# Performance work log

Hardware: AMD Instinct MI355X
Metric: run time of the kernel (lower is better)

Reference implementation:

```python
import jax, jax.numpy as jnp
import numpy as np

N_NODES = 50000
N_EDGES = 600000
BAG = 16
VOCAB = 10000
EMB = 128
HID = 128
N_CLASSES = 10
N_GRAPHS = 512
PAD_IDX = 1


def setup_inputs() -> dict:
    key = jax.random.key(0)
    ks = jax.random.split(key, 12)
    x_tokens = jax.random.randint(ks[0], (N_NODES, BAG), 0, VOCAB)
    src = jax.random.randint(ks[1], (N_EDGES,), 0, N_NODES)
    dst = jax.random.randint(ks[2], (N_EDGES,), 0, N_NODES)
    edge_index = jnp.stack([src, dst])
    batch = jnp.sort(jax.random.randint(ks[3], (N_NODES,), 0, N_GRAPHS))
    # rows 0,1 are zero in the original (weights[2:] filled from pretrained vectors)
    emb_table = (jax.random.normal(ks[4], (VOCAB, EMB)) * 0.02).at[:2].set(0.0)
    s = 1.0 / np.sqrt(EMB)
    w1_l = jax.random.normal(ks[5], (HID, EMB)) * s
    b1 = jnp.zeros((HID,), jnp.float32)
    w1_r = jax.random.normal(ks[6], (HID, EMB)) * s
    w2_l = jax.random.normal(ks[7], (HID, HID)) * s
    b2 = jnp.zeros((HID,), jnp.float32)
    w2_r = jax.random.normal(ks[8], (HID, HID)) * s
    w_out = jax.random.normal(ks[9], (N_CLASSES, HID)) * s
    b_out = jnp.zeros((N_CLASSES,), jnp.float32)
    return {"x_tokens": x_tokens, "edge_index": edge_index, "batch": batch,
            "emb_table": emb_table, "w1_l": w1_l, "b1": b1, "w1_r": w1_r,
            "w2_l": w2_l, "b2": b2, "w2_r": w2_r, "w_out": w_out, "b_out": b_out}


def _embedding_bag_mean(tokens, table):
    # nn.EmbeddingBag mode='mean' with padding_idx: padding tokens excluded from mean
    emb = table[tokens]                                  # [N, BAG, D]
    mask = (tokens != PAD_IDX)[..., None].astype(table.dtype)
    total = jnp.sum(emb * mask, axis=1)                  # [N, D]
    cnt = jnp.clip(jnp.sum(mask, axis=1), 1.0)           # [N, 1]
    return total / cnt


def _sage_conv(x, src, dst, w_l, b_l, w_r):
    # PyG SAGEConv: lin_l(mean_{j in N(i)} x_j) + lin_r(x_i); lin_r has no bias
    n = x.shape[0]
    msg_sum = jax.ops.segment_sum(x[src], dst, num_segments=n)           # [N, D]
    deg = jax.ops.segment_sum(jnp.ones((src.shape[0], 1), x.dtype), dst,
                              num_segments=n)                             # [N, 1]
    aggr = msg_sum / jnp.clip(deg, 1.0)
    return aggr @ w_l.T + b_l + x @ w_r.T


def reference(x_tokens, edge_index, batch, emb_table, w1_l, b1, w1_r,
              w2_l, b2, w2_r, w_out, b_out):
    src, dst = edge_index[0], edge_index[1]
    x = _embedding_bag_mean(x_tokens, emb_table)                 # [N, EMB]
    x = jax.nn.relu(_sage_conv(x, src, dst, w1_l, b1, w1_r))     # [N, HID]
    x = jax.nn.relu(_sage_conv(x, src, dst, w2_l, b2, w2_r))     # [N, HID]
    # global_mean_pool over graph ids
    g_sum = jax.ops.segment_sum(x, batch, num_segments=N_GRAPHS)
    g_cnt = jax.ops.segment_sum(jnp.ones((x.shape[0], 1), x.dtype), batch,
                                num_segments=N_GRAPHS)
    g = g_sum / jnp.clip(g_cnt, 1.0)                             # [G, HID]
    return g @ w_out.T + b_out                                   # [G, C]
```

## Files before the change

kernel.cpp:

```cpp
#include <hip/hip_runtime.h>
#include <hip/hip_bf16.h>

#define NN 50000
#define NE 600000
#define BAG 16
#define EMB 128
#define HID 128
#define NC 10
#define NG 512
#define PAD_IDX 1
#define VOCAB 10000
#define SLOTS 64
#define TPAIRS (VOCAB * EMB / 2)
#define WPAIRS (4 * HID * EMB / 2)
#define EMVB (NN / 16)
#define NCH1 293
#define RANGES 125
#define RNODES 400
#define QCAP 6400
#define NTILES ((NN + 127) / 128)

typedef __attribute__((ext_vector_type(8))) short v8s;
typedef __attribute__((ext_vector_type(4))) float v4f;

__device__ __forceinline__ float bflo(unsigned u) { return __uint_as_float(u << 16); }
__device__ __forceinline__ float bfhi(unsigned u) { return __uint_as_float(u & 0xffff0000u); }
__device__ __forceinline__ unsigned short f2bf(float f) {
    unsigned u = __float_as_uint(f);
    return (unsigned short)((u + 0x7fffu + ((u >> 16) & 1u)) >> 16);
}
__device__ __forceinline__ void acc8(float* a, v8s v) {
    unsigned* u = (unsigned*)&v;
#pragma unroll
    for (int j = 0; j < 4; j++) {
        a[2 * j] += bflo(u[j]);
        a[2 * j + 1] += bfhi(u[j]);
    }
}

__global__ void k_conv(const float* __restrict__ t, unsigned short* __restrict__ tb,
                       const float* __restrict__ w1l, const float* __restrict__ w1r,
                       const float* __restrict__ w2l, const float* __restrict__ w2r,
                       unsigned short* __restrict__ wbf, int* __restrict__ qtail,
                       float* __restrict__ gsum, float* __restrict__ gcnt) {
    int i = blockIdx.x * blockDim.x + threadIdx.x;
    if (i < RANGES) qtail[i] = 0;
    if (i < NG * HID) gsum[i] = 0.f;
    if (i < NG) gcnt[i] = 0.f;
    if (i < TPAIRS) {
        float2 v = *(const float2*)(t + (size_t)i * 2);
        unsigned lo = f2bf(v.x), hi = f2bf(v.y);
        *(unsigned*)(tb + (size_t)i * 2) = lo | (hi << 16);
    } else if (i < TPAIRS + WPAIRS) {
        int j = i - TPAIRS;
        int k = j * 2;
        int arr = k >> 14;
        int o = k & 16383;
        const float* w = (arr == 0) ? w1l : (arr == 1) ? w1r : (arr == 2) ? w2l : w2r;
        float2 v = *(const float2*)(w + o);
        unsigned lo = f2bf(v.x), hi = f2bf(v.y);
        *(unsigned*)(wbf + k) = lo | (hi << 16);
    }
}

__global__ __launch_bounds__(256) void k_scatem(const int* __restrict__ src,
                                                const int* __restrict__ dst,
                                                int* __restrict__ qtail,
                                                unsigned* __restrict__ queue,
                                                const int* __restrict__ tokens,
                                                const unsigned short* __restrict__ table,
                                                unsigned short* __restrict__ x0) {
    __shared__ int qcntL[RANGES];
    __shared__ unsigned qbufL[RANGES * 64];
    int b = blockIdx.x;
    int tid = threadIdx.x;

    if (b < NCH1) {
        for (int i = tid; i < RANGES; i += 256) qcntL[i] = 0;
        __syncthreads();
        int e0 = b * 2048 + tid * 8;
        if (e0 < NE) {
            int4 s0 = *((const int4*)(src + e0));
            int4 s1 = *((const int4*)(src + e0) + 1);
            int4 d0 = *((const int4*)(dst + e0));
            int4 d1 = *((const int4*)(dst + e0) + 1);
            int ss[8] = {s0.x, s0.y, s0.z, s0.w, s1.x, s1.y, s1.z, s1.w};
            int dd[8] = {d0.x, d0.y, d0.z, d0.w, d1.x, d1.y, d1.z, d1.w};
#pragma unroll
            for (int j = 0; j < 8; j++) {
                int q = dd[j] / RNODES;
                unsigned pk = ((unsigned)(dd[j] - q * RNODES) << 16) | (unsigned)ss[j];
                int pos = atomicAdd(&qcntL[q], 1);
                if (pos < 64) qbufL[q * 64 + pos] = pk;
            }
        }
        __syncthreads();
        if (tid < RANGES) {
            int n = qcntL[tid];
            if (n > 64) n = 64;
            int base = atomicAdd(&qtail[tid], n);
            if (base + n > QCAP) n = (QCAP - base > 0) ? QCAP - base : 0;
            unsigned* qp = queue + (size_t)tid * QCAP + base;
            for (int k = 0; k < n; k++) qp[k] = qbufL[tid * 64 + k];
        }
        return;
    }

    int sl = tid & 15;
    int node = (b - NCH1) * 16 + (tid >> 4);
    const int* tp = tokens + node * BAG;
    int tk[16];
    *(int4*)(tk) = *(const int4*)(tp);
    *(int4*)(tk + 4) = *(const int4*)(tp + 4);
    *(int4*)(tk + 8) = *(const int4*)(tp + 8);
    *(int4*)(tk + 12) = *(const int4*)(tp + 12);
    int c = 0;
#pragma unroll
    for (int t = 0; t < BAG; t++) c += (tk[t] != PAD_IDX);
    float a[8];
#pragma unroll
    for (int j = 0; j < 8; j++) a[j] = 0.f;
#pragma unroll
    for (int h = 0; h < 2; h++) {
        v8s v[8];
#pragma unroll
        for (int t = 0; t < 8; t++)
            v[t] = *(const v8s*)(table + (size_t)tk[h * 8 + t] * EMB + sl * 8);
#pragma unroll
        for (int t = 0; t < 8; t++) acc8(a, v[t]);
    }
    float inv = 1.0f / (float)(c > 0 ? c : 1);
    uint4 o;
    o.x = f2bf(a[0] * inv) | ((unsigned)f2bf(a[1] * inv) << 16);
    o.y = f2bf(a[2] * inv) | ((unsigned)f2bf(a[3] * inv) << 16);
    o.z = f2bf(a[4] * inv) | ((unsigned)f2bf(a[5] * inv) << 16);
    o.w = f2bf(a[6] * inv) | ((unsigned)f2bf(a[7] * inv) << 16);
    *(uint4*)(x0 + (size_t)node * EMB + sl * 8) = o;
}

__global__ __launch_bounds__(256) void k_csr(const int* __restrict__ qtail,
                                             const unsigned* __restrict__ queue,
                                             int* __restrict__ cnt,
                                             unsigned short* __restrict__ slots) {
    __shared__ int cntL[RNODES];
    __shared__ __align__(16) unsigned short slotsL[RNODES * SLOTS];
    int r = blockIdx.x, tid = threadIdx.x;
    for (int i = tid; i < RNODES; i += 256) cntL[i] = 0;
    __syncthreads();
    int n = qtail[r];
    if (n > QCAP) n = QCAP;
    const unsigned* qp = queue + (size_t)r * QCAP;
    for (int i = tid; i < n; i += 256) {
        unsigned u = qp[i];
        int dl = u >> 16;
        int p = atomicAdd(&cntL[dl], 1);
        if (p < SLOTS) slotsL[dl * SLOTS + p] = (unsigned short)(u & 0xffffu);
    }
    __syncthreads();
    uint4* gs = (uint4*)(slots + (size_t)r * RNODES * SLOTS);
    const uint4* ls = (const uint4*)slotsL;
    for (int i = tid; i < RNODES * SLOTS / 8; i += 256) gs[i] = ls[i];
    for (int i = tid; i < RNODES; i += 256) cnt[r * RNODES + i] = cntL[i];
}

__global__ __launch_bounds__(256) void k_aggr(const unsigned short* __restrict__ x,
                                              const int* __restrict__ cnt,
                                              const unsigned short* __restrict__ slots,
                                              unsigned short* __restrict__ aggr) {
    int node = blockIdx.x * 4 + (threadIdx.x >> 6);
    int lane = threadIdx.x & 63;
    if (node >= NN) return;
    int deg = cnt[node];
    int m = deg > SLOTS ? SLOTS : deg;
    int g = lane >> 4, sl = lane & 15;
    float a[8];
#pragma unroll
    for (int j = 0; j < 8; j++) a[j] = 0.f;
    int idx_l = slots[(size_t)node * SLOTS + ((lane < m) ? lane : 0)];
    int i = 0;
    for (; i + 8 <= m; i += 8) {
        int t0 = __shfl(idx_l, i + g, 64);
        int t1 = __shfl(idx_l, i + 4 + g, 64);
        v8s v0 = *(const v8s*)(x + (size_t)t0 * HID + sl * 8);
        v8s v1 = *(const v8s*)(x + (size_t)t1 * HID + sl * 8);
        acc8(a, v0);
        acc8(a, v1);
    }
    for (; i + 4 <= m; i += 4) {
        int t0 = __shfl(idx_l, i + g, 64);
        v8s v0 = *(const v8s*)(x + (size_t)t0 * HID + sl * 8);
        acc8(a, v0);
    }
    int rem = m - i;
    if (rem > 0) {
        int t0 = __shfl(idx_l, (g < rem) ? i + g : i, 64);
        v8s v0 = *(const v8s*)(x + (size_t)t0 * HID + sl * 8);
        if (g < rem) acc8(a, v0);
    }
#pragma unroll
    for (int j = 0; j < 8; j++) {
        a[j] += __shfl_xor(a[j], 16, 64);
        a[j] += __shfl_xor(a[j], 32, 64);
    }
    float inv = 1.0f / (float)(deg > 0 ? deg : 1);
    if (g == 0) {
        uint4 o;
        o.x = f2bf(a[0] * inv) | ((unsigned)f2bf(a[1] * inv) << 16);
        o.y = f2bf(a[2] * inv) | ((unsigned)f2bf(a[3] * inv) << 16);
        o.z = f2bf(a[4] * inv) | ((unsigned)f2bf(a[5] * inv) << 16);
        o.w = f2bf(a[6] * inv) | ((unsigned)f2bf(a[7] * inv) << 16);
        *(uint4*)(aggr + (size_t)node * HID + sl * 8) = o;
    }
}

__device__ __forceinline__ void sage_kloop(int row0, const unsigned short* __restrict__ xa,
                                           const unsigned short* __restrict__ xr,
                                           const unsigned short* __restrict__ wl,
                                           const unsigned short* __restrict__ wr,
                                           unsigned short* As, unsigned short* Bs,
                                           v4f acc[2][8]) {
    int tid = threadIdx.x;
    int wave = tid >> 6, lane = tid & 63;
    int q = lane >> 4, l16 = lane & 15;
    for (int kc = 0; kc < 8; kc++) {
        const unsigned short* Ag = (kc < 4) ? xa : xr;
        const unsigned short* Bg = (kc < 4) ? wl : wr;
        int koff = (kc & 3) * 32;
#pragma unroll
        for (int it = 0; it < 2; it++) {
            int seg = tid + it * 256;
            int r = seg >> 2, sg = seg & 3;
            int gr = row0 + r;
            if (gr > NN - 1) gr = NN - 1;
            v8s a = *(const v8s*)(Ag + (size_t)gr * HID + koff + sg * 8);
            *(v8s*)(As + r * 32 + sg * 8) = a;
            v8s b = *(const v8s*)(Bg + (size_t)r * HID + koff + sg * 8);
            *(v8s*)(Bs + r * 32 + sg * 8) = b;
        }
        __syncthreads();
        v8s a0 = *(const v8s*)(As + (wave * 32 + l16) * 32 + q * 8);
        v8s a1 = *(const v8s*)(As + (wave * 32 + 16 + l16) * 32 + q * 8);
#pragma unroll
        for (int nt = 0; nt < 8; nt++) {
            v8s b = *(const v8s*)(Bs + (nt * 16 + l16) * 32 + q * 8);
            acc[0][nt] = __builtin_amdgcn_mfma_f32_16x16x32_bf16(a0, b, acc[0][nt], 0, 0, 0);
            acc[1][nt] = __builtin_amdgcn_mfma_f32_16x16x32_bf16(a1, b, acc[1][nt], 0, 0, 0);
        }
        __syncthreads();
    }
}

__global__ __launch_bounds__(256) void k_sage(const unsigned short* __restrict__ xa,
                                              const unsigned short* __restrict__ xr,
                                              const unsigned short* __restrict__ wl,
                                              const unsigned short* __restrict__ wr,
                                              const float* __restrict__ bias,
                                              unsigned short* __restrict__ out) {
    __shared__ unsigned short As[128 * 32];
    __shared__ unsigned short Bs[128 * 32];
    int row0 = blockIdx.x * 128;
    v4f acc[2][8];
#pragma unroll
    for (int m = 0; m < 2; m++)
#pragma unroll
        for (int n = 0; n < 8; n++) acc[m][n] = (v4f){0.f, 0.f, 0.f, 0.f};
    sage_kloop(row0, xa, xr, wl, wr, As, Bs, acc);
    int tid = threadIdx.x;
    int wave = tid >> 6, lane = tid & 63;
    int q = lane >> 4, l16 = lane & 15;
#pragma unroll
    for (int nt = 0; nt < 8; nt++) {
        int col = nt * 16 + l16;
        float bv = bias[col];
#pragma unroll
        for (int mt = 0; mt < 2; mt++) {
#pragma unroll
            for (int r = 0; r < 4; r++) {
                int row = row0 + wave * 32 + mt * 16 + q * 4 + r;
                if (row < NN) {
                    float v = acc[mt][nt][r] + bv;
                    v = v > 0.f ? v : 0.f;
                    out[(size_t)row * HID + col] = f2bf(v);
                }
            }
        }
    }
}

__global__ __launch_bounds__(256) void k_sagepool(const unsigned short* __restrict__ xa,
                                                  const unsigned short* __restrict__ xr,
                                                  const unsigned short* __restrict__ wl,
                                                  const unsigned short* __restrict__ wr,
                                                  const float* __restrict__ bias,
                                                  const int* __restrict__ batch,
                                                  float* __restrict__ gsum,
                                                  float* __restrict__ gcnt) {
    __shared__ unsigned short smem[128 * 128];
    unsigned short* As = smem;
    unsigned short* Bs = smem + 128 * 32;
    int row0 = blockIdx.x * 128;
    v4f acc[2][8];
#pragma unroll
    for (int m = 0; m < 2; m++)
#pragma unroll
        for (int n = 0; n < 8; n++) acc[m][n] = (v4f){0.f, 0.f, 0.f, 0.f};
    sage_kloop(row0, xa, xr, wl, wr, As, Bs, acc);
    int tid = threadIdx.x;
    int wave = tid >> 6, lane = tid & 63;
    int q = lane >> 4, l16 = lane & 15;
#pragma unroll
    for (int nt = 0; nt < 8; nt++) {
        int col = nt * 16 + l16;
        float bv = bias[col];
#pragma unroll
        for (int mt = 0; mt < 2; mt++) {
#pragma unroll
            for (int r = 0; r < 4; r++) {
                int rl = wave * 32 + mt * 16 + q * 4 + r;
                float v = acc[mt][nt][r] + bv;
                v = v > 0.f ? v : 0.f;
                smem[rl * 128 + col] = f2bf(v);
            }
        }
    }
    __syncthreads();
    if (tid < 128) {
        int col = tid;
        int end = NN - row0;
        if (end > 128) end = 128;
        int cur = batch[row0];
        float acc_p = 0.f;
        int c = 0;
        for (int i = 0; i < end; i++) {
            int b = batch[row0 + i];
            if (b != cur) {
                atomicAdd(&gsum[cur * HID + col], acc_p);
                if (col == 0) atomicAdd(&gcnt[cur], (float)c);
                acc_p = 0.f;
                c = 0;
                cur = b;
            }
            acc_p += __uint_as_float(((unsigned)smem[i * 128 + col]) << 16);
            c++;
        }
        atomicAdd(&gsum[cur * HID + col], acc_p);
        if (col == 0) atomicAdd(&gcnt[cur], (float)c);
    }
}

__global__ __launch_bounds__(128) void k_final(const float* __restrict__ gsum,
                                               const float* __restrict__ gcnt,
                                               const float* __restrict__ w_out,
                                               const float* __restrict__ b_out,
                                               float* __restrict__ out) {
    __shared__ float mean[HID];
    int g = blockIdx.x, tid = threadIdx.x;
    mean[tid] = gsum[g * HID + tid] / fmaxf(gcnt[g], 1.0f);
    __syncthreads();
    if (tid < NC) {
        float s = b_out[tid];
#pragma unroll 16
        for (int d = 0; d < HID; d++) s += mean[d] * w_out[tid * HID + d];
        out[g * NC + tid] = s;
    }
}

extern "C" void kernel_launch(void* const* d_in, const int* in_sizes, int n_in,
                              void* d_out, int out_size, void* d_ws, size_t ws_size,
                              hipStream_t stream) {
    const int* x_tokens = (const int*)d_in[0];
    const int* edge = (const int*)d_in[1];
    const int* batch = (const int*)d_in[2];
    const float* emb_table = (const float*)d_in[3];
    const float* w1l = (const float*)d_in[4];
    const float* b1 = (const float*)d_in[5];
    const float* w1r = (const float*)d_in[6];
    const float* w2l = (const float*)d_in[7];
    const float* b2 = (const float*)d_in[8];
    const float* w2r = (const float*)d_in[9];
    const float* w_out = (const float*)d_in[10];
    const float* b_out = (const float*)d_in[11];
    float* out = (float*)d_out;

    char* ws = (char*)d_ws;
    size_t off = 0;
    auto alloc = [&](size_t bytes) {
        void* p = ws + off;
        off += (bytes + 255) & ~(size_t)255;
        return p;
    };
    int* cnt = (int*)alloc(NN * 4);
    unsigned short* slots = (unsigned short*)alloc((size_t)NN * SLOTS * 2);
    unsigned short* wbf = (unsigned short*)alloc(4 * HID * EMB * 2);
    float* gsum = (float*)alloc(NG * HID * 4);
    float* gcnt = (float*)alloc(NG * 4);
    unsigned short* x0 = (unsigned short*)alloc((size_t)NN * EMB * 2);
    unsigned short* x1 = (unsigned short*)alloc((size_t)NN * HID * 2);
    unsigned short* aggrb = (unsigned short*)alloc((size_t)NN * HID * 2);
    unsigned* queue = (unsigned*)alloc((size_t)RANGES * QCAP * 4);
    int* qtail = (int*)alloc(RANGES * 4);
    unsigned short* table_bf = x1;

    const int* srcp = edge;
    const int* dstp = edge + NE;

    k_conv<<<(TPAIRS + WPAIRS + 255) / 256, 256, 0, stream>>>(
        emb_table, table_bf, w1l, w1r, w2l, w2r, wbf, qtail, gsum, gcnt);
    k_scatem<<<NCH1 + EMVB, 256, 0, stream>>>(srcp, dstp, qtail, queue, x_tokens,
                                              table_bf, x0);
    k_csr<<<RANGES, 256, 0, stream>>>(qtail, queue, cnt, slots);
    k_aggr<<<(NN + 3) / 4, 256, 0, stream>>>(x0, cnt, slots, aggrb);
    k_sage<<<NTILES, 256, 0, stream>>>(aggrb, x0, wbf, wbf + 16384, b1, x1);
    k_aggr<<<(NN + 3) / 4, 256, 0, stream>>>(x1, cnt, slots, aggrb);
    k_sagepool<<<NTILES, 256, 0, stream>>>(aggrb, x1, wbf + 32768, wbf + 49152, b2,
                                           batch, gsum, gcnt);
    k_final<<<NG, 128, 0, stream>>>(gsum, gcnt, w_out, b_out, out);
}
```

Measured before the change: 197.8 us.

## Process two nodes per wave in aggregation with zero-row padded neighbor slots

Each wave in the neighbor-mean aggregation now handles two nodes at once, interleaving their gathers to raise memory-level parallelism per wave. The CSR build pads each node's slot list up to a multiple of 8 with a sentinel index pointing at an extra zero row appended to the feature buffers. This removes the remainder loops and branchy tail handling. The cost is extra zero-row loads and a sentinel row that must be zeroed every call, and the grid size now assumes the node count divides by 8.

```diff
diff --git a/kernel.cpp b/kernel.cpp
--- a/kernel.cpp
+++ b/kernel.cpp
@@ -42,11 +42,16 @@
                        const float* __restrict__ w1l, const float* __restrict__ w1r,
                        const float* __restrict__ w2l, const float* __restrict__ w2r,
                        unsigned short* __restrict__ wbf, int* __restrict__ qtail,
-                       float* __restrict__ gsum, float* __restrict__ gcnt) {
+                       float* __restrict__ gsum, float* __restrict__ gcnt,
+                       unsigned short* __restrict__ x0, unsigned short* __restrict__ x1) {
     int i = blockIdx.x * blockDim.x + threadIdx.x;
     if (i < RANGES) qtail[i] = 0;
     if (i < NG * HID) gsum[i] = 0.f;
     if (i < NG) gcnt[i] = 0.f;
+    if (i < 64) {
+        ((unsigned*)(x0 + (size_t)NN * EMB))[i] = 0;
+        ((unsigned*)(x1 + (size_t)NN * HID))[i] = 0;
+    }
     if (i < TPAIRS) {
         float2 v = *(const float2*)(t + (size_t)i * 2);
         unsigned lo = f2bf(v.x), hi = f2bf(v.y);
@@ -157,6 +162,14 @@
         if (p < SLOTS) slotsL[dl * SLOTS + p] = (unsigned short)(u & 0xffffu);
     }
     __syncthreads();
+    for (int i = tid; i < RNODES; i += 256) {
+        int d = cntL[i];
+        if (d > SLOTS) d = SLOTS;
+        int d8 = (d + 7) & ~7;
+        if (d8 > SLOTS) d8 = SLOTS;
+        for (int p = d; p < d8; p++) slotsL[i * SLOTS + p] = (unsigned short)NN;
+    }
+    __syncthreads();
     uint4* gs = (uint4*)(slots + (size_t)r * RNODES * SLOTS);
     const uint4* ls = (const uint4*)slotsL;
     for (int i = tid; i < RNODES * SLOTS / 8; i += 256) gs[i] = ls[i];
@@ -167,49 +180,73 @@
                                               const int* __restrict__ cnt,
                                               const unsigned short* __restrict__ slots,
                                               unsigned short* __restrict__ aggr) {
-    int node = blockIdx.x * 4 + (threadIdx.x >> 6);
+    int wv = threadIdx.x >> 6;
     int lane = threadIdx.x & 63;
-    if (node >= NN) return;
-    int deg = cnt[node];
-    int m = deg > SLOTS ? SLOTS : deg;
+    int n0 = (blockIdx.x * 4 + wv) * 2;
+    int n1 = n0 + 1;
     int g = lane >> 4, sl = lane & 15;
-    float a[8];
-#pragma unroll
-    for (int j = 0; j < 8; j++) a[j] = 0.f;
-    int idx_l = slots[(size_t)node * SLOTS + ((lane < m) ? lane : 0)];
-    int i = 0;
-    for (; i + 8 <= m; i += 8) {
-        int t0 = __shfl(idx_l, i + g, 64);
-        int t1 = __shfl(idx_l, i + 4 + g, 64);
-        v8s v0 = *(const v8s*)(x + (size_t)t0 * HID + sl * 8);
-        v8s v1 = *(const v8s*)(x + (size_t)t1 * HID + sl * 8);
-        acc8(a, v0);
-        acc8(a, v1);
-    }
-    for (; i + 4 <= m; i += 4) {
-        int t0 = __shfl(idx_l, i + g, 64);
-        v8s v0 = *(const v8s*)(x + (size_t)t0 * HID + sl * 8);
-        acc8(a, v0);
-    }
-    int rem = m - i;
-    if (rem > 0) {
-        int t0 = __shfl(idx_l, (g < rem) ? i + g : i, 64);
-        v8s v0 = *(const v8s*)(x + (size_t)t0 * HID + sl * 8);
-        if (g < rem) acc8(a, v0);
-    }
+    int deg0 = cnt[n0], deg1 = cnt[n1];
+    int m0 = deg0 > SLOTS ? SLOTS : deg0;
+    int m1 = deg1 > SLOTS ? SLOTS : deg1;
+    int m80 = (m0 + 7) & ~7;
+    int m81 = (m1 + 7) & ~7;
+    int idx0 = slots[(size_t)n0 * SLOTS + lane];
+    int idx1 = slots[(size_t)n1 * SLOTS + lane];
+    float a0[8], a1[8];
 #pragma unroll
     for (int j = 0; j < 8; j++) {
-        a[j] += __shfl_xor(a[j], 16, 64);
-        a[j] += __shfl_xor(a[j], 32, 64);
-    }
-    float inv = 1.0f / (float)(deg > 0 ? deg : 1);
+        a0[j] = 0.f;
+        a1[j] = 0.f;
+    }
+    int mm = m80 > m81 ? m80 : m81;
+#pragma unroll 2
+    for (int i = 0; i < mm; i += 8) {
+        bool c0 = (i < m80), c1 = (i < m81);
+        v8s w0, w1, w2, w3;
+        if (c0) {
+            int t00 = __shfl(idx0, i + g, 64);
+            int t01 = __shfl(idx0, i + 4 + g, 64);
+            w0 = *(const v8s*)(x + (size_t)t00 * HID + sl * 8);
+            w1 = *(const v8s*)(x + (size_t)t01 * HID + sl * 8);
+        }
+        if (c1) {
+            int t10 = __shfl(idx1, i + g, 64);
+            int t11 = __shfl(idx1, i + 4 + g, 64);
+            w2 = *(const v8s*)(x + (size_t)t10 * HID + sl * 8);
+            w3 = *(const v8s*)(x + (size_t)t11 * HID + sl * 8);
+        }
+        if (c0) {
+            acc8(a0, w0);
+            acc8(a0, w1);
+        }
+        if (c1) {
+            acc8(a1, w2);
+            acc8(a1, w3);
+        }
+    }
+#pragma unroll
+    for (int j = 0; j < 8; j++) {
+        a0[j] += __shfl_xor(a0[j], 16, 64);
+        a0[j] += __shfl_xor(a0[j], 32, 64);
+        a1[j] += __shfl_xor(a1[j], 16, 64);
+        a1[j] += __shfl_xor(a1[j], 32, 64);
+    }
     if (g == 0) {
+        float inv = 1.0f / (float)(deg0 > 0 ? deg0 : 1);
         uint4 o;
-        o.x = f2bf(a[0] * inv) | ((unsigned)f2bf(a[1] * inv) << 16);
-        o.y = f2bf(a[2] * inv) | ((unsigned)f2bf(a[3] * inv) << 16);
-        o.z = f2bf(a[4] * inv) | ((unsigned)f2bf(a[5] * inv) << 16);
-        o.w = f2bf(a[6] * inv) | ((unsigned)f2bf(a[7] * inv) << 16);
-        *(uint4*)(aggr + (size_t)node * HID + sl * 8) = o;
+        o.x = f2bf(a0[0] * inv) | ((unsigned)f2bf(a0[1] * inv) << 16);
+        o.y = f2bf(a0[2] * inv) | ((unsigned)f2bf(a0[3] * inv) << 16);
+        o.z = f2bf(a0[4] * inv) | ((unsigned)f2bf(a0[5] * inv) << 16);
+        o.w = f2bf(a0[6] * inv) | ((unsigned)f2bf(a0[7] * inv) << 16);
+        *(uint4*)(aggr + (size_t)n0 * HID + sl * 8) = o;
+    } else if (g == 1) {
+        float inv = 1.0f / (float)(deg1 > 0 ? deg1 : 1);
+        uint4 o;
+        o.x = f2bf(a1[0] * inv) | ((unsigned)f2bf(a1[1] * inv) << 16);
+        o.y = f2bf(a1[2] * inv) | ((unsigned)f2bf(a1[3] * inv) << 16);
+        o.z = f2bf(a1[4] * inv) | ((unsigned)f2bf(a1[5] * inv) << 16);
+        o.w = f2bf(a1[6] * inv) | ((unsigned)f2bf(a1[7] * inv) << 16);
+        *(uint4*)(aggr + (size_t)n1 * HID + sl * 8) = o;
     }
 }
 
@@ -394,8 +431,8 @@
     unsigned short* wbf = (unsigned short*)alloc(4 * HID * EMB * 2);
     float* gsum = (float*)alloc(NG * HID * 4);
     float* gcnt = (float*)alloc(NG * 4);
-    unsigned short* x0 = (unsigned short*)alloc((size_t)NN * EMB * 2);
-    unsigned short* x1 = (unsigned short*)alloc((size_t)NN * HID * 2);
+    unsigned short* x0 = (unsigned short*)alloc((size_t)(NN + 1) * EMB * 2);
+    unsigned short* x1 = (unsigned short*)alloc((size_t)(NN + 1) * HID * 2);
     unsigned short* aggrb = (unsigned short*)alloc((size_t)NN * HID * 2);
     unsigned* queue = (unsigned*)alloc((size_t)RANGES * QCAP * 4);
     int* qtail = (int*)alloc(RANGES * 4);
@@ -405,13 +442,13 @@
     const int* dstp = edge + NE;
 
     k_conv<<<(TPAIRS + WPAIRS + 255) / 256, 256, 0, stream>>>(
-        emb_table, table_bf, w1l, w1r, w2l, w2r, wbf, qtail, gsum, gcnt);
+        emb_table, table_bf, w1l, w1r, w2l, w2r, wbf, qtail, gsum, gcnt, x0, x1);
     k_scatem<<<NCH1 + EMVB, 256, 0, stream>>>(srcp, dstp, qtail, queue, x_tokens,
                                               table_bf, x0);
     k_csr<<<RANGES, 256, 0, stream>>>(qtail, queue, cnt, slots);
-    k_aggr<<<(NN + 3) / 4, 256, 0, stream>>>(x0, cnt, slots, aggrb);
+    k_aggr<<<NN / 8, 256, 0, stream>>>(x0, cnt, slots, aggrb);
     k_sage<<<NTILES, 256, 0, stream>>>(aggrb, x0, wbf, wbf + 16384, b1, x1);
-    k_aggr<<<(NN + 3) / 4, 256, 0, stream>>>(x1, cnt, slots, aggrb);
+    k_aggr<<<NN / 8, 256, 0, stream>>>(x1, cnt, slots, aggrb);
     k_sagepool<<<NTILES, 256, 0, stream>>>(aggrb, x1, wbf + 32768, wbf + 49152, b2,
                                            batch, gsum, gcnt);
     k_final<<<NG, 128, 0, stream>>>(gsum, gcnt, w_out, b_out, out);
```

Result: no change. 198.0 us (+0.1%).
